# Performance work log

Measured on AMD Instinct MI355X. Metric: run time of the kernel, lower is better.

Reference implementation:

```python
import jax, jax.numpy as jnp
import numpy as np

N_CLS = 8192
FEAT_DIM = 512
BATCH = 1024
PROTO_M = 0.95
TEMPERATURE = 0.1
BASE_TEMPERATURE = 0.1
EPS = 1e-12  # F.normalize eps


def setup_inputs() -> dict:
    key = jax.random.key(0)
    k1, k2, k3 = jax.random.split(key, 3)
    features = jax.random.normal(k1, (BATCH, FEAT_DIM), dtype=jnp.float32)
    features = features / jnp.maximum(jnp.linalg.norm(features, axis=1, keepdims=True), EPS)
    labels = jax.random.randint(k2, (BATCH,), 0, N_CLS, dtype=jnp.int64 if jax.config.jax_enable_x64 else jnp.int32)
    prototypes = jax.random.normal(k3, (N_CLS, FEAT_DIM), dtype=jnp.float32)
    prototypes = prototypes / jnp.maximum(jnp.linalg.norm(prototypes, axis=1, keepdims=True), EPS)
    return {"features": features, "labels": labels, "prototypes": prototypes}


def _l2norm_vec(v):
    # F.normalize(v, dim=0) for a 1-D vector
    return v / jnp.maximum(jnp.linalg.norm(v), EPS)


def reference(features, labels, prototypes):
    # --- sequential per-sample EMA prototype update (order matters) ---
    def step(protos, fl):
        f, l = fl
        new_p = _l2norm_vec(protos[l] * PROTO_M + f * (1.0 - PROTO_M))
        return protos.at[l].set(new_p), None

    protos, _ = jax.lax.scan(step, prototypes, (features, labels))

    # --- dispersion loss over prototype pairs ---
    logits = (protos @ protos.T) / TEMPERATURE            # [n_cls, n_cls]
    n = protos.shape[0]
    mask = 1.0 - jnp.eye(n, dtype=logits.dtype)           # off-diagonal pairs
    # log of mean exp over negatives (exactly the original, non-stabilized, form;
    # prototypes are unit-norm so |logits| <= 1/T and exp is safe)
    mean_prob_neg = jnp.log((mask * jnp.exp(logits)).sum(axis=1) / mask.sum(axis=1))
    # original drops NaN rows; with n_cls > 1 mask.sum(1) == n_cls-1 > 0 so none occur
    loss = (TEMPERATURE / BASE_TEMPERATURE) * mean_prob_neg.mean()
    return loss
```

## Files before the change

kernel.cpp:

```cpp
#include <hip/hip_runtime.h>
#include <hip/hip_fp8.h>
#include <stdint.h>

#define N_CLS 8192
#define FEAT  512
#define BATCH 1024
#define NTI   32
#define NTJ   64
#define NBLK  1056
#define NSLOT 16
#define SLOTB 12288

typedef __attribute__((ext_vector_type(4))) float f32x4;

__device__ inline unsigned char f2fp8(float x) {
    __hip_fp8_e4m3 q(x);
    return q.__x;
}

__global__ __launch_bounds__(256) void ema_kernel(
    const float* __restrict__ features, const int* __restrict__ labels,
    const float* __restrict__ protos,
    unsigned char* __restrict__ Phi8, float* __restrict__ rowsum) {
    const int row  = blockIdx.x * 4 + (threadIdx.x >> 6);
    const int lane = threadIdx.x & 63;
    if (lane == 0) rowsum[row] = 0.f;

    float p[8];
    #pragma unroll
    for (int j = 0; j < 8; ++j) p[j] = protos[(size_t)row * FEAT + j * 64 + lane];

    for (int c = 0; c < BATCH / 64; ++c) {
        int lab = labels[c * 64 + lane];
        unsigned long long m = __ballot(lab == row);
        while (m) {
            int b = __builtin_ctzll(m);
            m &= m - 1;
            int s = c * 64 + b;
            float ss = 0.f;
            #pragma unroll
            for (int j = 0; j < 8; ++j) {
                float f = features[(size_t)s * FEAT + j * 64 + lane];
                p[j] = p[j] * 0.95f + f * 0.05f;
                ss += p[j] * p[j];
            }
            #pragma unroll
            for (int off = 32; off; off >>= 1) ss += __shfl_xor(ss, off);
            float inv = 1.0f / fmaxf(sqrtf(ss), 1e-12f);
            #pragma unroll
            for (int j = 0; j < 8; ++j) p[j] *= inv;
        }
    }
    #pragma unroll
    for (int j = 0; j < 8; ++j)
        Phi8[(size_t)row * FEAT + j * 64 + lane] = f2fp8(p[j]);
}

__global__ __launch_bounds__(512, 4) void gemm_disp_kernel(
    const unsigned char* __restrict__ Phi8, float* __restrict__ rowsum) {
    __shared__ __align__(16) char smem[3 * SLOTB];

    int bid = blockIdx.x;
    int u = (bid & 7) * (NBLK / 8) + (bid >> 3);
    int i = 0;
    while (u >= NTJ - 2 * i) { u -= NTJ - 2 * i; ++i; }
    const int j = 2 * i + u;
    const bool diagovl = ((j >> 1) == i);

    const int w    = threadIdx.x >> 6;
    const int lane = threadIdx.x & 63;
    const int wr = w >> 1, wc = w & 1;
    const int h = lane >> 4;
    const int r = lane & 15;
    const int rseg = ((h >> 1) ^ ((r >> 2) & 1)) * 16 + (h & 1) * 8;

    const int Ibase = i * 256, Jbase = j * 128;

    f32x4 acc[4][4];
    #pragma unroll
    for (int m = 0; m < 4; ++m)
        #pragma unroll
        for (int n = 0; n < 4; ++n) acc[m][n] = (f32x4){0.f, 0.f, 0.f, 0.f};

    const int sg = (lane & 1) ^ ((lane >> 3) & 1);
    const unsigned char* gA =
        Phi8 + (size_t)(Ibase + w * 32 + (lane >> 1)) * FEAT + sg * 16;
    const unsigned char* gB =
        Phi8 + (size_t)(Jbase + (w & 3) * 32 + (lane >> 1)) * FEAT + sg * 16;

#define STAGE(s)                                                              \
    {                                                                         \
        char* la = smem + ((s) % 3) * SLOTB + w * 1024;                       \
        __builtin_amdgcn_global_load_lds(                                     \
            (const __attribute__((address_space(1))) void*)(gA + (s) * 32),   \
            (__attribute__((address_space(3))) void*)la, 16, 0, 0);           \
        if (w >= 4) {                                                         \
            char* lb = smem + ((s) % 3) * SLOTB + 8192 + (w & 3) * 1024;      \
            __builtin_amdgcn_global_load_lds(                                 \
                (const __attribute__((address_space(1))) void*)(gB + (s) * 32),\
                (__attribute__((address_space(3))) void*)lb, 16, 0, 0);       \
        }                                                                     \
    }

#define SLOT(s, TAIL)                                                         \
    {                                                                         \
        const char* As = smem + ((s) % 3) * SLOTB;                            \
        const char* Bs = As + 8192;                                           \
        long a0, a1, a2, a3, b0, b1, b2, b3;                                  \
        b0 = *(const long*)(Bs + (wc * 64 +  0 + r) * 32 + rseg);             \
        b1 = *(const long*)(Bs + (wc * 64 + 16 + r) * 32 + rseg);             \
        b2 = *(const long*)(Bs + (wc * 64 + 32 + r) * 32 + rseg);             \
        b3 = *(const long*)(Bs + (wc * 64 + 48 + r) * 32 + rseg);             \
        a0 = *(const long*)(As + (wr * 64 +  0 + r) * 32 + rseg);             \
        a1 = *(const long*)(As + (wr * 64 + 16 + r) * 32 + rseg);             \
        a2 = *(const long*)(As + (wr * 64 + 32 + r) * 32 + rseg);             \
        a3 = *(const long*)(As + (wr * 64 + 48 + r) * 32 + rseg);             \
        __builtin_amdgcn_s_setprio(1);                                        \
        acc[0][0] = __builtin_amdgcn_mfma_f32_16x16x32_fp8_fp8(a0, b0, acc[0][0], 0, 0, 0); \
        acc[1][0] = __builtin_amdgcn_mfma_f32_16x16x32_fp8_fp8(a1, b0, acc[1][0], 0, 0, 0); \
        acc[2][0] = __builtin_amdgcn_mfma_f32_16x16x32_fp8_fp8(a2, b0, acc[2][0], 0, 0, 0); \
        acc[3][0] = __builtin_amdgcn_mfma_f32_16x16x32_fp8_fp8(a3, b0, acc[3][0], 0, 0, 0); \
        acc[0][1] = __builtin_amdgcn_mfma_f32_16x16x32_fp8_fp8(a0, b1, acc[0][1], 0, 0, 0); \
        acc[1][1] = __builtin_amdgcn_mfma_f32_16x16x32_fp8_fp8(a1, b1, acc[1][1], 0, 0, 0); \
        acc[2][1] = __builtin_amdgcn_mfma_f32_16x16x32_fp8_fp8(a2, b1, acc[2][1], 0, 0, 0); \
        acc[3][1] = __builtin_amdgcn_mfma_f32_16x16x32_fp8_fp8(a3, b1, acc[3][1], 0, 0, 0); \
        acc[0][2] = __builtin_amdgcn_mfma_f32_16x16x32_fp8_fp8(a0, b2, acc[0][2], 0, 0, 0); \
        acc[1][2] = __builtin_amdgcn_mfma_f32_16x16x32_fp8_fp8(a1, b2, acc[1][2], 0, 0, 0); \
        acc[2][2] = __builtin_amdgcn_mfma_f32_16x16x32_fp8_fp8(a2, b2, acc[2][2], 0, 0, 0); \
        acc[3][2] = __builtin_amdgcn_mfma_f32_16x16x32_fp8_fp8(a3, b2, acc[3][2], 0, 0, 0); \
        acc[0][3] = __builtin_amdgcn_mfma_f32_16x16x32_fp8_fp8(a0, b3, acc[0][3], 0, 0, 0); \
        acc[1][3] = __builtin_amdgcn_mfma_f32_16x16x32_fp8_fp8(a1, b3, acc[1][3], 0, 0, 0); \
        acc[2][3] = __builtin_amdgcn_mfma_f32_16x16x32_fp8_fp8(a2, b3, acc[2][3], 0, 0, 0); \
        acc[3][3] = __builtin_amdgcn_mfma_f32_16x16x32_fp8_fp8(a3, b3, acc[3][3], 0, 0, 0); \
        __builtin_amdgcn_s_setprio(0);                                        \
        TAIL                                                                  \
    }

#define WAITC                                                                 \
    if (w < 4) asm volatile("s_waitcnt vmcnt(1)" ::: "memory");               \
    else       asm volatile("s_waitcnt vmcnt(2)" ::: "memory");

#define TAIL_MID(s)                                                           \
    STAGE((s) + 2)                                                            \
    WAITC                                                                     \
    __builtin_amdgcn_s_barrier();
#define TAIL_14                                                               \
    asm volatile("s_waitcnt vmcnt(0)" ::: "memory");                          \
    __builtin_amdgcn_s_barrier();
#define TAIL_15

    STAGE(0) STAGE(1)
    WAITC
    __builtin_amdgcn_s_barrier();

    SLOT(0,  TAIL_MID(0))  SLOT(1,  TAIL_MID(1))  SLOT(2,  TAIL_MID(2))
    SLOT(3,  TAIL_MID(3))  SLOT(4,  TAIL_MID(4))  SLOT(5,  TAIL_MID(5))
    SLOT(6,  TAIL_MID(6))  SLOT(7,  TAIL_MID(7))  SLOT(8,  TAIL_MID(8))
    SLOT(9,  TAIL_MID(9))  SLOT(10, TAIL_MID(10)) SLOT(11, TAIL_MID(11))
    SLOT(12, TAIL_MID(12)) SLOT(13, TAIL_MID(13))
    SLOT(14, TAIL_14)
    SLOT(15, TAIL_15)

    #pragma unroll
    for (int m = 0; m < 4; ++m)
        #pragma unroll
        for (int n = 0; n < 4; ++n)
            #pragma unroll
            for (int q = 0; q < 4; ++q) {
                float v = __expf(acc[m][n][q] * 10.0f);
                if (diagovl &&
                    (Ibase + wr * 64 + m * 16 + h * 4 + q) ==
                    (Jbase + wc * 64 + n * 16 + r))
                    v = 0.f;
                acc[m][n][q] = v;
            }

    #pragma unroll
    for (int m = 0; m < 4; ++m) {
        float rs[4];
        #pragma unroll
        for (int q = 0; q < 4; ++q)
            rs[q] = acc[m][0][q] + acc[m][1][q] + acc[m][2][q] + acc[m][3][q];
        #pragma unroll
        for (int q = 0; q < 4; ++q)
            #pragma unroll
            for (int off = 1; off < 16; off <<= 1) rs[q] += __shfl_xor(rs[q], off);
        if (r == 0) {
            #pragma unroll
            for (int q = 0; q < 4; ++q)
                atomicAdd(&rowsum[Ibase + wr * 64 + m * 16 + h * 4 + q], rs[q]);
        }
    }

    if (!diagovl) {
        #pragma unroll
        for (int n = 0; n < 4; ++n) {
            float cs = 0.f;
            #pragma unroll
            for (int m = 0; m < 4; ++m)
                #pragma unroll
                for (int q = 0; q < 4; ++q) cs += acc[m][n][q];
            cs += __shfl_xor(cs, 16);
            cs += __shfl_xor(cs, 32);
            if (lane < 16)
                atomicAdd(&rowsum[Jbase + wc * 64 + n * 16 + r], cs);
        }
    }
}

__global__ __launch_bounds__(512) void loss_kernel(
    const float* __restrict__ rowsum, float* __restrict__ out) {
    __shared__ float red[8];
    float s = 0.f;
    for (int i = threadIdx.x; i < N_CLS; i += 512)
        s += logf(rowsum[i] * (1.0f / (float)(N_CLS - 1)));
    #pragma unroll
    for (int off = 32; off; off >>= 1) s += __shfl_xor(s, off);
    if ((threadIdx.x & 63) == 0) red[threadIdx.x >> 6] = s;
    __syncthreads();
    if (threadIdx.x == 0) {
        float tot = 0.f;
        #pragma unroll
        for (int i = 0; i < 8; ++i) tot += red[i];
        out[0] = tot * (1.0f / (float)N_CLS);
    }
}

extern "C" void kernel_launch(void* const* d_in, const int* in_sizes, int n_in,
                              void* d_out, int out_size, void* d_ws, size_t ws_size,
                              hipStream_t stream) {
    (void)in_sizes; (void)n_in; (void)out_size; (void)ws_size;
    const float* features = (const float*)d_in[0];
    const int*   labels   = (const int*)d_in[1];
    const float* protos   = (const float*)d_in[2];
    float* out = (float*)d_out;

    unsigned char* Phi8 = (unsigned char*)d_ws;
    float* rowsum = (float*)(Phi8 + (size_t)N_CLS * FEAT);

    ema_kernel<<<N_CLS / 4, 256, 0, stream>>>(features, labels, protos, Phi8, rowsum);
    gemm_disp_kernel<<<NBLK, 512, 0, stream>>>(Phi8, rowsum);
    loss_kernel<<<1, 512, 0, stream>>>(rowsum, out);
}
```

Baseline: 69.42 us.

## Double K-slice per pipeline stage to halve barriers in fp8 GEMM

Result: faster. 58.83 us (-15.3%).

```diff
diff --git a/kernel.cpp b/kernel.cpp
--- a/kernel.cpp
+++ b/kernel.cpp
@@ -8,10 +8,11 @@
 #define NTI   32
 #define NTJ   64
 #define NBLK  1056
-#define NSLOT 16
-#define SLOTB 12288
+#define NSLOT 8
+#define SLOTB 24576
 
 typedef __attribute__((ext_vector_type(4))) float f32x4;
+typedef __attribute__((ext_vector_type(2))) long longx2;
 
 __device__ inline unsigned char f2fp8(float x) {
     __hip_fp8_e4m3 q(x);
@@ -72,7 +73,7 @@
     const int wr = w >> 1, wc = w & 1;
     const int h = lane >> 4;
     const int r = lane & 15;
-    const int rseg = ((h >> 1) ^ ((r >> 2) & 1)) * 16 + (h & 1) * 8;
+    const int rseg = (h ^ ((r >> 1) & 3)) * 16;
 
     const int Ibase = i * 256, Jbase = j * 128;
 
@@ -82,84 +83,75 @@
         #pragma unroll
         for (int n = 0; n < 4; ++n) acc[m][n] = (f32x4){0.f, 0.f, 0.f, 0.f};
 
-    const int sg = (lane & 1) ^ ((lane >> 3) & 1);
+    const int srow = lane >> 2;
+    const int sseg = (lane & 3) ^ ((lane >> 3) & 3);
     const unsigned char* gA =
-        Phi8 + (size_t)(Ibase + w * 32 + (lane >> 1)) * FEAT + sg * 16;
+        Phi8 + (size_t)(Ibase + w * 32 + srow) * FEAT + sseg * 16;
     const unsigned char* gB =
-        Phi8 + (size_t)(Jbase + (w & 3) * 32 + (lane >> 1)) * FEAT + sg * 16;
+        Phi8 + (size_t)(Jbase + w * 16 + srow) * FEAT + sseg * 16;
 
 #define STAGE(s)                                                              \
     {                                                                         \
-        char* la = smem + ((s) % 3) * SLOTB + w * 1024;                       \
+        char* base = smem + ((s) % 3) * SLOTB;                                \
         __builtin_amdgcn_global_load_lds(                                     \
-            (const __attribute__((address_space(1))) void*)(gA + (s) * 32),   \
-            (__attribute__((address_space(3))) void*)la, 16, 0, 0);           \
-        if (w >= 4) {                                                         \
-            char* lb = smem + ((s) % 3) * SLOTB + 8192 + (w & 3) * 1024;      \
-            __builtin_amdgcn_global_load_lds(                                 \
-                (const __attribute__((address_space(1))) void*)(gB + (s) * 32),\
-                (__attribute__((address_space(3))) void*)lb, 16, 0, 0);       \
-        }                                                                     \
-    }
+            (const __attribute__((address_space(1))) void*)(gA + (s) * 64),   \
+            (__attribute__((address_space(3))) void*)(base + w * 2048),       \
+            16, 0, 0);                                                        \
+        __builtin_amdgcn_global_load_lds(                                     \
+            (const __attribute__((address_space(1))) void*)(gA + 16 * FEAT + (s) * 64), \
+            (__attribute__((address_space(3))) void*)(base + w * 2048 + 1024),\
+            16, 0, 0);                                                        \
+        __builtin_amdgcn_global_load_lds(                                     \
+            (const __attribute__((address_space(1))) void*)(gB + (s) * 64),   \
+            (__attribute__((address_space(3))) void*)(base + 16384 + w * 1024),\
+            16, 0, 0);                                                        \
+    }
+
+#define MF8(ai, bi, mi, ni)                                                   \
+    acc[mi][ni] = __builtin_amdgcn_mfma_f32_16x16x32_fp8_fp8(                 \
+        ai[0], bi[0], acc[mi][ni], 0, 0, 0);                                  \
+    acc[mi][ni] = __builtin_amdgcn_mfma_f32_16x16x32_fp8_fp8(                 \
+        ai[1], bi[1], acc[mi][ni], 0, 0, 0);
 
 #define SLOT(s, TAIL)                                                         \
     {                                                                         \
         const char* As = smem + ((s) % 3) * SLOTB;                            \
-        const char* Bs = As + 8192;                                           \
-        long a0, a1, a2, a3, b0, b1, b2, b3;                                  \
-        b0 = *(const long*)(Bs + (wc * 64 +  0 + r) * 32 + rseg);             \
-        b1 = *(const long*)(Bs + (wc * 64 + 16 + r) * 32 + rseg);             \
-        b2 = *(const long*)(Bs + (wc * 64 + 32 + r) * 32 + rseg);             \
-        b3 = *(const long*)(Bs + (wc * 64 + 48 + r) * 32 + rseg);             \
-        a0 = *(const long*)(As + (wr * 64 +  0 + r) * 32 + rseg);             \
-        a1 = *(const long*)(As + (wr * 64 + 16 + r) * 32 + rseg);             \
-        a2 = *(const long*)(As + (wr * 64 + 32 + r) * 32 + rseg);             \
-        a3 = *(const long*)(As + (wr * 64 + 48 + r) * 32 + rseg);             \
+        const char* Bs = As + 16384;                                          \
+        longx2 a0, a1, a2, a3, b0, b1, b2, b3;                                \
+        b0 = *(const longx2*)(Bs + (wc * 64 +  0 + r) * 64 + rseg);           \
+        b1 = *(const longx2*)(Bs + (wc * 64 + 16 + r) * 64 + rseg);           \
+        b2 = *(const longx2*)(Bs + (wc * 64 + 32 + r) * 64 + rseg);           \
+        b3 = *(const longx2*)(Bs + (wc * 64 + 48 + r) * 64 + rseg);           \
+        a0 = *(const longx2*)(As + (wr * 64 +  0 + r) * 64 + rseg);           \
+        a1 = *(const longx2*)(As + (wr * 64 + 16 + r) * 64 + rseg);           \
+        a2 = *(const longx2*)(As + (wr * 64 + 32 + r) * 64 + rseg);           \
+        a3 = *(const longx2*)(As + (wr * 64 + 48 + r) * 64 + rseg);           \
         __builtin_amdgcn_s_setprio(1);                                        \
-        acc[0][0] = __builtin_amdgcn_mfma_f32_16x16x32_fp8_fp8(a0, b0, acc[0][0], 0, 0, 0); \
-        acc[1][0] = __builtin_amdgcn_mfma_f32_16x16x32_fp8_fp8(a1, b0, acc[1][0], 0, 0, 0); \
-        acc[2][0] = __builtin_amdgcn_mfma_f32_16x16x32_fp8_fp8(a2, b0, acc[2][0], 0, 0, 0); \
-        acc[3][0] = __builtin_amdgcn_mfma_f32_16x16x32_fp8_fp8(a3, b0, acc[3][0], 0, 0, 0); \
-        acc[0][1] = __builtin_amdgcn_mfma_f32_16x16x32_fp8_fp8(a0, b1, acc[0][1], 0, 0, 0); \
-        acc[1][1] = __builtin_amdgcn_mfma_f32_16x16x32_fp8_fp8(a1, b1, acc[1][1], 0, 0, 0); \
-        acc[2][1] = __builtin_amdgcn_mfma_f32_16x16x32_fp8_fp8(a2, b1, acc[2][1], 0, 0, 0); \
-        acc[3][1] = __builtin_amdgcn_mfma_f32_16x16x32_fp8_fp8(a3, b1, acc[3][1], 0, 0, 0); \
-        acc[0][2] = __builtin_amdgcn_mfma_f32_16x16x32_fp8_fp8(a0, b2, acc[0][2], 0, 0, 0); \
-        acc[1][2] = __builtin_amdgcn_mfma_f32_16x16x32_fp8_fp8(a1, b2, acc[1][2], 0, 0, 0); \
-        acc[2][2] = __builtin_amdgcn_mfma_f32_16x16x32_fp8_fp8(a2, b2, acc[2][2], 0, 0, 0); \
-        acc[3][2] = __builtin_amdgcn_mfma_f32_16x16x32_fp8_fp8(a3, b2, acc[3][2], 0, 0, 0); \
-        acc[0][3] = __builtin_amdgcn_mfma_f32_16x16x32_fp8_fp8(a0, b3, acc[0][3], 0, 0, 0); \
-        acc[1][3] = __builtin_amdgcn_mfma_f32_16x16x32_fp8_fp8(a1, b3, acc[1][3], 0, 0, 0); \
-        acc[2][3] = __builtin_amdgcn_mfma_f32_16x16x32_fp8_fp8(a2, b3, acc[2][3], 0, 0, 0); \
-        acc[3][3] = __builtin_amdgcn_mfma_f32_16x16x32_fp8_fp8(a3, b3, acc[3][3], 0, 0, 0); \
+        MF8(a0, b0, 0, 0) MF8(a1, b0, 1, 0) MF8(a2, b0, 2, 0) MF8(a3, b0, 3, 0) \
+        MF8(a0, b1, 0, 1) MF8(a1, b1, 1, 1) MF8(a2, b1, 2, 1) MF8(a3, b1, 3, 1) \
+        MF8(a0, b2, 0, 2) MF8(a1, b2, 1, 2) MF8(a2, b2, 2, 2) MF8(a3, b2, 3, 2) \
+        MF8(a0, b3, 0, 3) MF8(a1, b3, 1, 3) MF8(a2, b3, 2, 3) MF8(a3, b3, 3, 3) \
         __builtin_amdgcn_s_setprio(0);                                        \
         TAIL                                                                  \
     }
 
-#define WAITC                                                                 \
-    if (w < 4) asm volatile("s_waitcnt vmcnt(1)" ::: "memory");               \
-    else       asm volatile("s_waitcnt vmcnt(2)" ::: "memory");
-
 #define TAIL_MID(s)                                                           \
     STAGE((s) + 2)                                                            \
-    WAITC                                                                     \
+    asm volatile("s_waitcnt vmcnt(3)" ::: "memory");                          \
     __builtin_amdgcn_s_barrier();
-#define TAIL_14                                                               \
+#define TAIL_6                                                                \
     asm volatile("s_waitcnt vmcnt(0)" ::: "memory");                          \
     __builtin_amdgcn_s_barrier();
-#define TAIL_15
+#define TAIL_7
 
     STAGE(0) STAGE(1)
-    WAITC
+    asm volatile("s_waitcnt vmcnt(3)" ::: "memory");
     __builtin_amdgcn_s_barrier();
 
-    SLOT(0,  TAIL_MID(0))  SLOT(1,  TAIL_MID(1))  SLOT(2,  TAIL_MID(2))
-    SLOT(3,  TAIL_MID(3))  SLOT(4,  TAIL_MID(4))  SLOT(5,  TAIL_MID(5))
-    SLOT(6,  TAIL_MID(6))  SLOT(7,  TAIL_MID(7))  SLOT(8,  TAIL_MID(8))
-    SLOT(9,  TAIL_MID(9))  SLOT(10, TAIL_MID(10)) SLOT(11, TAIL_MID(11))
-    SLOT(12, TAIL_MID(12)) SLOT(13, TAIL_MID(13))
-    SLOT(14, TAIL_14)
-    SLOT(15, TAIL_15)
+    SLOT(0, TAIL_MID(0)) SLOT(1, TAIL_MID(1)) SLOT(2, TAIL_MID(2))
+    SLOT(3, TAIL_MID(3)) SLOT(4, TAIL_MID(4)) SLOT(5, TAIL_MID(5))
+    SLOT(6, TAIL_6)
+    SLOT(7, TAIL_7)
 
     #pragma unroll
     for (int m = 0; m < 4; ++m)
```
